# Kernel optimization log

Measured on AMD Instinct MI355X. Metric: run time of the kernel, lower is better.

Reference implementation:

```python
import jax, jax.numpy as jnp
import numpy as np
from jax.ops import segment_sum, segment_max

N_NODES = 100000
N_EDGES = 1600000
IN, HID, OUT = 256, 64, 40
NEG_SLOPE = 0.2  # DGL GATConv default


def setup_inputs() -> dict:
    key = jax.random.key(0)
    ks = jax.random.split(key, 12)
    feat = jax.random.normal(ks[0], (N_NODES, IN), dtype=jnp.float32)
    src = jax.random.randint(ks[1], (N_EDGES,), 0, N_NODES)
    dst = jax.random.randint(ks[2], (N_EDGES,), 0, N_NODES)
    def xavier(k, shape):
        fan = sum(shape)
        return jax.random.normal(k, shape, dtype=jnp.float32) * jnp.sqrt(2.0 / fan)
    return {
        "feat": feat, "src": src, "dst": dst,
        "W1": xavier(ks[3], (IN, HID)),  "b1": jnp.zeros((HID,), jnp.float32),
        "al1": xavier(ks[4], (HID,)),    "ar1": xavier(ks[5], (HID,)),
        "W2": xavier(ks[6], (HID, OUT)), "b2": jnp.zeros((OUT,), jnp.float32),
        "al2": xavier(ks[7], (OUT,)),    "ar2": xavier(ks[8], (OUT,)),
    }


def gat_layer(x, W, b, attn_l, attn_r, src, dst, n):
    # z: [N, F_out] projected features
    z = x @ W
    el = z @ attn_l          # [N] source attention logits
    er = z @ attn_r          # [N] destination attention logits
    e = jax.nn.leaky_relu(el[src] + er[dst], NEG_SLOPE)  # [E]
    # segment (per-destination) softmax over incoming edges
    m = segment_max(e, dst, num_segments=n)              # [N]
    w = jnp.exp(e - m[dst])                              # [E]
    s = segment_sum(w, dst, num_segments=n)              # [N]
    alpha = w / s[dst]                                   # [E]
    # scatter-add aggregation of alpha * z[src]
    out = segment_sum(alpha[:, None] * z[src], dst, num_segments=n)
    return out + b


def reference(feat, src, dst, W1, b1, al1, ar1, W2, b2, al2, ar2):
    n = feat.shape[0]
    h = gat_layer(feat, W1, b1, al1, ar1, src, dst, n)
    h = jax.nn.relu(h)  # dropout is identity in eval mode
    h = gat_layer(h, W2, b2, al2, ar2, src, dst, n)
    return jax.nn.log_softmax(h, axis=-1)  # [N, out_size]
```

## Files before the change

### kernel.cpp

```cpp
#include <hip/hip_runtime.h>
#include <math.h>

constexpr int NN   = 100000;
constexpr int NE   = 1600000;
constexpr int FIN  = 256;
constexpr int HID  = 64;
constexpr int FOUT = 40;
constexpr float SLOPE = 0.2f;
constexpr int NBUCK = (NN + 127) / 128;
constexpr int TILE_A = 2048;
constexpr int NWG_A = (NE + TILE_A - 1) / TILE_A;
constexpr int NT_GEMM = (NN + 63) / 64;
constexpr int AK = 264;
constexpr int HB = 64;
constexpr int HIST_EPB = 4096;
constexpr int NWG_H = (NE + HIST_EPB - 1) / HIST_EPB;

typedef short  short8  __attribute__((ext_vector_type(8)));
typedef float  floatx4 __attribute__((ext_vector_type(4)));

__device__ inline unsigned short f2bf(float x) {
    union { float f; unsigned int u; } c; c.f = x;
    unsigned int u = c.u;
    return (unsigned short)((u + 0x7FFF + ((u >> 16) & 1)) >> 16);
}

__device__ inline float readlane_f(float v, int l) {
    return __int_as_float(__builtin_amdgcn_readlane(__float_as_int(v), l));
}

__device__ inline void scan_buckets(const int* __restrict__ gcnt,
                                    int* __restrict__ bofs,
                                    int* __restrict__ tsum, int t)
{
    int i0 = 4 * t;
    int c0 = (i0 + 0 < NBUCK) ? gcnt[i0 + 0] : 0;
    int c1 = (i0 + 1 < NBUCK) ? gcnt[i0 + 1] : 0;
    int c2 = (i0 + 2 < NBUCK) ? gcnt[i0 + 2] : 0;
    int c3 = (i0 + 3 < NBUCK) ? gcnt[i0 + 3] : 0;
    int s = c0 + c1 + c2 + c3;
    tsum[t] = s;
    __syncthreads();
    for (int off = 1; off < 256; off <<= 1) {
        int x = (t >= off) ? tsum[t - off] : 0;
        __syncthreads();
        tsum[t] += x;
        __syncthreads();
    }
    int e0 = tsum[t] - s;
    if (i0 + 0 <= NBUCK) bofs[i0 + 0] = e0;
    if (i0 + 1 <= NBUCK) bofs[i0 + 1] = e0 + c0;
    if (i0 + 2 <= NBUCK) bofs[i0 + 2] = e0 + c0 + c1;
    if (i0 + 3 <= NBUCK) bofs[i0 + 3] = e0 + c0 + c1 + c2;
    __syncthreads();
}

__global__ __launch_bounds__(256) void prep_kernel(
    const float* __restrict__ W1, unsigned short* __restrict__ W1T,
    const float* __restrict__ W2, const float* __restrict__ al2,
    const float* __restrict__ ar2,
    float* __restrict__ wl2, float* __restrict__ wr2,
    const int* __restrict__ dst, int* __restrict__ bcnt)
{
    const int t = threadIdx.x;
    if (blockIdx.x < HB) {
        int idx = blockIdx.x * 256 + t;
        if (idx < FIN * HID) {
            int k = idx >> 6, n = idx & 63;
            W1T[n * FIN + k] = f2bf(W1[idx]);
        }
        if (blockIdx.x == 0 && t < HID) {
            int k = t;
            float a = 0.f, b = 0.f;
            #pragma unroll 8
            for (int j = 0; j < FOUT; ++j) {
                float wv = W2[k * FOUT + j];
                a += wv * al2[j]; b += wv * ar2[j];
            }
            wl2[k] = a; wr2[k] = b;
        }
    } else {
        __shared__ int hist[NBUCK];
        for (int i = t; i < NBUCK; i += 256) hist[i] = 0;
        __syncthreads();
        int base = (blockIdx.x - HB) * HIST_EPB + t * 16;
        #pragma unroll
        for (int k = 0; k < 4; ++k) {
            int idx = base + 4 * k;
            if (idx < NE) {
                const int4 d4 = *(const int4*)&dst[idx];
                atomicAdd(&hist[d4.x >> 7], 1); atomicAdd(&hist[d4.y >> 7], 1);
                atomicAdd(&hist[d4.z >> 7], 1); atomicAdd(&hist[d4.w >> 7], 1);
            }
        }
        __syncthreads();
        for (int i = t; i < NBUCK; i += 256) {
            int hv = hist[i];
            if (hv) atomicAdd(&bcnt[i], hv);
        }
    }
}

__global__ __launch_bounds__(256) void mega_kernel(
    const float* __restrict__ feat, const unsigned short* __restrict__ W1T,
    const float* __restrict__ al, const float* __restrict__ ar,
    const int* __restrict__ src, const int* __restrict__ dst,
    const int* __restrict__ bcnt, int* __restrict__ cur0,
    int* __restrict__ ebuck,
    _Float16* __restrict__ z, float* __restrict__ el, float* __restrict__ er)
{
    __shared__ int smem4[8448];
    const int t = threadIdx.x;

    if (blockIdx.x < NT_GEMM) {
        unsigned short* sBT = (unsigned short*)smem4;
        const int ntile = blockIdx.x * 64;

        const int w  = t >> 6;
        const int l  = t & 63;
        const int lr = l & 15;
        const int q  = l >> 4;
        const int m0 = 16 * w;

        int n = ntile + m0 + lr; if (n >= NN) n = NN - 1;
        const float* __restrict__ arow = feat + (size_t)n * FIN;

        float4 fa[8], fb[8];
        #pragma unroll
        for (int kc = 0; kc < 8; ++kc) {
            const int koff = kc * 32 + 8 * q;
            fa[kc] = *(const float4*)(arow + koff);
            fb[kc] = *(const float4*)(arow + koff + 4);
        }

        #pragma unroll
        for (int i = 0; i < 8; ++i) {
            int g = t + 256 * i;
            int row = g >> 5, c8 = g & 31;
            *(uint4*)&sBT[row * AK + 8 * c8] = *(const uint4*)&W1T[row * FIN + 8 * c8];
        }
        __syncthreads();

        floatx4 acc[4];
        #pragma unroll
        for (int tile = 0; tile < 4; ++tile) acc[tile] = 0.f;

        #pragma unroll
        for (int kc = 0; kc < 8; ++kc) {
            const int koff = kc * 32 + 8 * q;
            short8 av;
            av[0] = (short)f2bf(fa[kc].x); av[1] = (short)f2bf(fa[kc].y);
            av[2] = (short)f2bf(fa[kc].z); av[3] = (short)f2bf(fa[kc].w);
            av[4] = (short)f2bf(fb[kc].x); av[5] = (short)f2bf(fb[kc].y);
            av[6] = (short)f2bf(fb[kc].z); av[7] = (short)f2bf(fb[kc].w);
            #pragma unroll
            for (int tile = 0; tile < 4; ++tile) {
                const short8 bv = *(const short8*)(sBT + (16 * tile + lr) * AK + koff);
                acc[tile] = __builtin_amdgcn_mfma_f32_16x16x32_bf16(av, bv, acc[tile], 0, 0, 0);
            }
        }

        float aln[4], arn[4];
        #pragma unroll
        for (int tile = 0; tile < 4; ++tile) {
            aln[tile] = al[16 * tile + lr];
            arn[tile] = ar[16 * tile + lr];
        }
        #pragma unroll
        for (int r = 0; r < 4; ++r) {
            int mg = ntile + m0 + 4 * q + r;
            float pl = 0.f, pr = 0.f;
            #pragma unroll
            for (int tile = 0; tile < 4; ++tile) {
                float zv = acc[tile][r];
                pl += zv * aln[tile]; pr += zv * arn[tile];
            }
            #pragma unroll
            for (int off = 8; off >= 1; off >>= 1) {
                pl += __shfl_xor(pl, off);
                pr += __shfl_xor(pr, off);
            }
            if (mg < NN) {
                #pragma unroll
                for (int tile = 0; tile < 4; ++tile)
                    z[(size_t)mg * HID + 16 * tile + lr] = (_Float16)acc[tile][r];
                if (lr == 0) { el[mg] = pl; er[mg] = pr; }
            }
        }
    } else {
        int* hist = smem4;
        int* bofs = smem4 + NBUCK;
        int* tsum = smem4 + 2 * NBUCK + 1;
        int* lcur = smem4 + 2 * NBUCK + 1 + 256;
        const int blk = blockIdx.x - NT_GEMM;
        const int e0 = blk * TILE_A;
        const int e1 = (e0 + TILE_A < NE) ? e0 + TILE_A : NE;

        for (int i = t; i < NBUCK; i += 256) hist[i] = 0;
        scan_buckets(bcnt, bofs, tsum, t);
        for (int e = e0 + t; e < e1; e += 256)
            atomicAdd(&hist[dst[e] >> 7], 1);
        __syncthreads();
        for (int i = t; i < NBUCK; i += 256) {
            int hv = hist[i];
            if (hv) lcur[i] = bofs[i] + atomicAdd(&cur0[i], hv);
        }
        __syncthreads();
        for (int e = e0 + t; e < e1; e += 256) {
            int d = dst[e], s_ = src[e];
            int p = atomicAdd(&lcur[d >> 7], 1);
            ebuck[p] = (s_ << 7) | (d & 127);
        }
    }
}

__global__ __launch_bounds__(256) void partB_kernel(
    const int* __restrict__ bcnt, const int* __restrict__ ebuck,
    int* __restrict__ row_ptr, int* __restrict__ esrc)
{
    __shared__ int bofs[NBUCK + 1];
    __shared__ int tsum[256];
    __shared__ int sdeg[128];
    __shared__ int sscan[128];
    __shared__ int scur[128];
    const int b = blockIdx.x;
    const int n0 = b << 7;
    const int t = threadIdx.x;

    if (t < 128) sdeg[t] = 0;
    scan_buckets(bcnt, bofs, tsum, t);
    const int r0 = bofs[b], r1 = bofs[b + 1];

    for (int e = r0 + t; e < r1; e += 256)
        atomicAdd(&sdeg[ebuck[e] & 127], 1);
    __syncthreads();

    if (t < 128) sscan[t] = sdeg[t];
    __syncthreads();
    for (int off = 1; off < 128; off <<= 1) {
        int x = (t < 128 && t >= off) ? sscan[t - off] : 0;
        __syncthreads();
        if (t < 128) sscan[t] += x;
        __syncthreads();
    }
    if (t < 128) {
        int excl = sscan[t] - sdeg[t];
        if (n0 + t < NN) row_ptr[n0 + t] = r0 + excl;
        scur[t] = r0 + excl;
    }
    if (b == NBUCK - 1 && t == 0) row_ptr[NN] = NE;
    __syncthreads();

    for (int e = r0 + t; e < r1; e += 256) {
        int pk = ebuck[e];
        int p = atomicAdd(&scur[pk & 127], 1);
        esrc[p] = pk >> 7;
    }
}

template<bool FIRST>
__global__ __launch_bounds__(256) void gat_gather_kernel(
    const int* __restrict__ row_ptr, const int* __restrict__ esrc,
    const float* __restrict__ el, const float* __restrict__ er,
    const _Float16* __restrict__ zin, const float* __restrict__ b1,
    const float* __restrict__ wl2, const float* __restrict__ wr2,
    _Float16* __restrict__ hout, _Float16* __restrict__ haggout,
    float* __restrict__ el2, float* __restrict__ er2)
{
    const int w = threadIdx.x >> 6, lane = threadIdx.x & 63;
    const int d = blockIdx.x * 4 + w;
    const int r0 = row_ptr[d], r1 = row_ptr[d + 1];
    const int cnt = r1 - r0;
    const float erd = er[d];

    float accv = 0.f;
    float s = 0.f;

    if (cnt <= 64) {
        int sn = 0; float v = -INFINITY;
        if (lane < cnt) {
            sn = esrc[r0 + lane];
            v = el[sn] + erd;
            v = (v >= 0.f) ? v : SLOPE * v;
        }
        float m = v;
        #pragma unroll
        for (int off = 32; off >= 1; off >>= 1) m = fmaxf(m, __shfl_xor(m, off));
        float wv = (lane < cnt) ? __expf(v - m) : 0.f;
        s = wv;
        #pragma unroll
        for (int off = 32; off >= 1; off >>= 1) s += __shfl_xor(s, off);
        {
            int j = 0;
            for (; j + 8 <= cnt; j += 8) {
                float a0 = 0.f, a1 = 0.f;
                #pragma unroll
                for (int qq = 0; qq < 8; qq += 2) {
                    float w0 = readlane_f(wv, j + qq);
                    int   s0 = __builtin_amdgcn_readlane(sn, j + qq);
                    float w1 = readlane_f(wv, j + qq + 1);
                    int   s1 = __builtin_amdgcn_readlane(sn, j + qq + 1);
                    a0 += w0 * (float)zin[(size_t)s0 * HID + lane];
                    a1 += w1 * (float)zin[(size_t)s1 * HID + lane];
                }
                accv += a0 + a1;
            }
            for (; j < cnt; ++j) {
                float w0 = readlane_f(wv, j);
                int   s0 = __builtin_amdgcn_readlane(sn, j);
                accv += w0 * (float)zin[(size_t)s0 * HID + lane];
            }
        }
    } else {
        float m = -INFINITY;
        for (int e = r0 + lane; e < r1; e += 64) {
            float v = el[esrc[e]] + erd;
            v = (v >= 0.f) ? v : SLOPE * v;
            m = fmaxf(m, v);
        }
        #pragma unroll
        for (int off = 32; off >= 1; off >>= 1) m = fmaxf(m, __shfl_xor(m, off));
        for (int base = r0; base < r1; base += 64) {
            int e = base + lane;
            float wv = 0.f; int sn = 0;
            if (e < r1) {
                sn = esrc[e];
                float v = el[sn] + erd;
                v = (v >= 0.f) ? v : SLOPE * v;
                wv = __expf(v - m);
            }
            s += wv;
            int c = r1 - base; if (c > 64) c = 64;
            {
                int j = 0;
                for (; j + 4 <= c; j += 4) {
                    float a0 = 0.f, a1 = 0.f;
                    #pragma unroll
                    for (int qq = 0; qq < 4; qq += 2) {
                        float w0 = readlane_f(wv, j + qq);
                        int   s0 = __builtin_amdgcn_readlane(sn, j + qq);
                        float w1 = readlane_f(wv, j + qq + 1);
                        int   s1 = __builtin_amdgcn_readlane(sn, j + qq + 1);
                        a0 += w0 * (float)zin[(size_t)s0 * HID + lane];
                        a1 += w1 * (float)zin[(size_t)s1 * HID + lane];
                    }
                    accv += a0 + a1;
                }
                for (; j < c; ++j) {
                    float w0 = readlane_f(wv, j);
                    int   s0 = __builtin_amdgcn_readlane(sn, j);
                    accv += w0 * (float)zin[(size_t)s0 * HID + lane];
                }
            }
        }
        #pragma unroll
        for (int off = 32; off >= 1; off >>= 1) s += __shfl_xor(s, off);
    }

    float res = (cnt > 0) ? (accv / s) : 0.f;

    if (FIRST) {
        float hval = res + b1[lane];
        hval = (hval > 0.f) ? hval : 0.f;
        hout[(size_t)d * HID + lane] = (_Float16)hval;
        float pl = hval * wl2[lane];
        float pr = hval * wr2[lane];
        #pragma unroll
        for (int off = 32; off >= 1; off >>= 1) {
            pl += __shfl_xor(pl, off); pr += __shfl_xor(pr, off);
        }
        if (lane == 0) { el2[d] = pl; er2[d] = pr; }
    } else {
        haggout[(size_t)d * HID + lane] = (_Float16)res;
    }
}

__global__ __launch_bounds__(256) void out_kernel(
    const _Float16* __restrict__ hagg, const float* __restrict__ W2,
    const float* __restrict__ b2, float* __restrict__ out)
{
    __shared__ float sh[4][64];
    const int w = threadIdx.x >> 6, lane = threadIdx.x & 63;
    const int n = blockIdx.x * 4 + w;
    sh[w][lane] = (float)hagg[(size_t)n * HID + lane];
    __syncthreads();
    float acc = 0.f;
    if (lane < FOUT) {
        #pragma unroll 8
        for (int k = 0; k < HID; ++k) acc += sh[w][k] * W2[k * FOUT + lane];
    }
    float v = (lane < FOUT) ? acc + b2[lane] : -INFINITY;
    float mx = v;
    #pragma unroll
    for (int off = 32; off >= 1; off >>= 1) mx = fmaxf(mx, __shfl_xor(mx, off));
    float ex = (lane < FOUT) ? __expf(v - mx) : 0.f;
    float sm = ex;
    #pragma unroll
    for (int off = 32; off >= 1; off >>= 1) sm += __shfl_xor(sm, off);
    if (lane < FOUT) out[(size_t)n * FOUT + lane] = v - mx - __logf(sm);
}

extern "C" void kernel_launch(void* const* d_in, const int* in_sizes, int n_in,
                              void* d_out, int out_size, void* d_ws, size_t ws_size,
                              hipStream_t stream) {
    const float* feat = (const float*)d_in[0];
    const int*   src  = (const int*)d_in[1];
    const int*   dst  = (const int*)d_in[2];
    const float* W1   = (const float*)d_in[3];
    const float* b1   = (const float*)d_in[4];
    const float* al1  = (const float*)d_in[5];
    const float* ar1  = (const float*)d_in[6];
    const float* W2   = (const float*)d_in[7];
    const float* b2   = (const float*)d_in[8];
    const float* al2  = (const float*)d_in[9];
    const float* ar2  = (const float*)d_in[10];
    float* out = (float*)d_out;

    char* p = (char*)d_ws;
    _Float16* hagg = (_Float16*)p;
    _Float16* z1   = (_Float16*)p;  p += (size_t)NN * HID * 2;
    _Float16* h    = (_Float16*)p;  p += (size_t)NN * HID * 2;
    float* el1   = (float*)p;     p += (size_t)NN * 4;
    float* er1   = (float*)p;     p += (size_t)NN * 4;
    float* el2   = (float*)p;     p += (size_t)NN * 4;
    float* er2   = (float*)p;     p += (size_t)NN * 4;
    float* wl2   = (float*)p;     p += HID * 4;
    float* wr2   = (float*)p;     p += HID * 4;
    int*   bcnt  = (int*)p;       p += NBUCK * 4;
    int*   cur0  = (int*)p;       p += NBUCK * 4;
    int*   rowp  = (int*)p;       p += (NN + 1) * 4;
    int*   esrc  = (int*)p;       p += (size_t)NE * 4;
    int*   ebuck = (int*)p;       p += (size_t)NE * 4;
    unsigned short* w1t = (unsigned short*)p;

    hipMemsetAsync(bcnt, 0, 2 * NBUCK * sizeof(int), stream);

    prep_kernel<<<HB + NWG_H, 256, 0, stream>>>(
        W1, w1t, W2, al2, ar2, wl2, wr2, dst, bcnt);

    mega_kernel<<<NT_GEMM + NWG_A, 256, 0, stream>>>(
        feat, w1t, al1, ar1, src, dst, bcnt, cur0, ebuck, z1, el1, er1);

    partB_kernel<<<NBUCK, 256, 0, stream>>>(bcnt, ebuck, rowp, esrc);

    gat_gather_kernel<true><<<NN / 4, 256, 0, stream>>>(
        rowp, esrc, el1, er1, z1, b1, wl2, wr2, h, nullptr, el2, er2);

    gat_gather_kernel<false><<<NN / 4, 256, 0, stream>>>(
        rowp, esrc, el2, er2, h, nullptr, nullptr, nullptr,
        nullptr, hagg, nullptr, nullptr);

    out_kernel<<<NN / 4, 256, 0, stream>>>(hagg, W2, b2, out);
}
```

Before: 419.7 us.

## Double GEMM rows per workgroup in fused kernel to amortize W1 LDS staging

Each GEMM workgroup now processes 128 nodes instead of 64, computing two sets of MFMA accumulators that share the same W1 B-fragment loaded from LDS. This halves the number of W1 staging copies and GEMM blocks, and the feat loads are now interleaved with compute per k-chunk rather than all prefetched up front. The trade-off is fewer GEMM blocks, which lowers parallelism, and more accumulator registers per thread. The lcur write is also made unconditional, a minor branch cleanup.

After: 417.4 us. Within noise of the previous version (-0.5%).

```diff
diff --git a/kernel.cpp b/kernel.cpp
--- a/kernel.cpp
+++ b/kernel.cpp
@@ -10,7 +10,7 @@
 constexpr int NBUCK = (NN + 127) / 128;
 constexpr int TILE_A = 2048;
 constexpr int NWG_A = (NE + TILE_A - 1) / TILE_A;
-constexpr int NT_GEMM = (NN + 63) / 64;
+constexpr int NT_GEMM = (NN + 127) / 128;
 constexpr int AK = 264;
 constexpr int HB = 64;
 constexpr int HIST_EPB = 4096;
@@ -114,7 +114,15 @@
 
     if (blockIdx.x < NT_GEMM) {
         unsigned short* sBT = (unsigned short*)smem4;
-        const int ntile = blockIdx.x * 64;
+        const int ntile = blockIdx.x * 128;
+
+        #pragma unroll
+        for (int i = 0; i < 8; ++i) {
+            int g = t + 256 * i;
+            int row = g >> 5, c8 = g & 31;
+            *(uint4*)&sBT[row * AK + 8 * c8] = *(const uint4*)&W1T[row * FIN + 8 * c8];
+        }
+        __syncthreads();
 
         const int w  = t >> 6;
         const int l  = t & 63;
@@ -122,41 +130,36 @@
         const int q  = l >> 4;
         const int m0 = 16 * w;
 
-        int n = ntile + m0 + lr; if (n >= NN) n = NN - 1;
-        const float* __restrict__ arow = feat + (size_t)n * FIN;
-
-        float4 fa[8], fb[8];
+        int n1 = ntile + m0 + lr; if (n1 >= NN) n1 = NN - 1;
+        int n2 = ntile + 64 + m0 + lr; if (n2 >= NN) n2 = NN - 1;
+        const float* __restrict__ arow1 = feat + (size_t)n1 * FIN;
+        const float* __restrict__ arow2 = feat + (size_t)n2 * FIN;
+
+        floatx4 acc1[4], acc2[4];
+        #pragma unroll
+        for (int tile = 0; tile < 4; ++tile) { acc1[tile] = 0.f; acc2[tile] = 0.f; }
+
         #pragma unroll
         for (int kc = 0; kc < 8; ++kc) {
             const int koff = kc * 32 + 8 * q;
-            fa[kc] = *(const float4*)(arow + koff);
-            fb[kc] = *(const float4*)(arow + koff + 4);
-        }
-
-        #pragma unroll
-        for (int i = 0; i < 8; ++i) {
-            int g = t + 256 * i;
-            int row = g >> 5, c8 = g & 31;
-            *(uint4*)&sBT[row * AK + 8 * c8] = *(const uint4*)&W1T[row * FIN + 8 * c8];
-        }
-        __syncthreads();
-
-        floatx4 acc[4];
-        #pragma unroll
-        for (int tile = 0; tile < 4; ++tile) acc[tile] = 0.f;
-
-        #pragma unroll
-        for (int kc = 0; kc < 8; ++kc) {
-            const int koff = kc * 32 + 8 * q;
-            short8 av;
-            av[0] = (short)f2bf(fa[kc].x); av[1] = (short)f2bf(fa[kc].y);
-            av[2] = (short)f2bf(fa[kc].z); av[3] = (short)f2bf(fa[kc].w);
-            av[4] = (short)f2bf(fb[kc].x); av[5] = (short)f2bf(fb[kc].y);
-            av[6] = (short)f2bf(fb[kc].z); av[7] = (short)f2bf(fb[kc].w);
+            const float4 fa1 = *(const float4*)(arow1 + koff);
+            const float4 fb1 = *(const float4*)(arow1 + koff + 4);
+            const float4 fa2 = *(const float4*)(arow2 + koff);
+            const float4 fb2 = *(const float4*)(arow2 + koff + 4);
+            short8 av1, av2;
+            av1[0] = (short)f2bf(fa1.x); av1[1] = (short)f2bf(fa1.y);
+            av1[2] = (short)f2bf(fa1.z); av1[3] = (short)f2bf(fa1.w);
+            av1[4] = (short)f2bf(fb1.x); av1[5] = (short)f2bf(fb1.y);
+            av1[6] = (short)f2bf(fb1.z); av1[7] = (short)f2bf(fb1.w);
+            av2[0] = (short)f2bf(fa2.x); av2[1] = (short)f2bf(fa2.y);
+            av2[2] = (short)f2bf(fa2.z); av2[3] = (short)f2bf(fa2.w);
+            av2[4] = (short)f2bf(fb2.x); av2[5] = (short)f2bf(fb2.y);
+            av2[6] = (short)f2bf(fb2.z); av2[7] = (short)f2bf(fb2.w);
             #pragma unroll
             for (int tile = 0; tile < 4; ++tile) {
                 const short8 bv = *(const short8*)(sBT + (16 * tile + lr) * AK + koff);
-                acc[tile] = __builtin_amdgcn_mfma_f32_16x16x32_bf16(av, bv, acc[tile], 0, 0, 0);
+                acc1[tile] = __builtin_amdgcn_mfma_f32_16x16x32_bf16(av1, bv, acc1[tile], 0, 0, 0);
+                acc2[tile] = __builtin_amdgcn_mfma_f32_16x16x32_bf16(av2, bv, acc2[tile], 0, 0, 0);
             }
         }
 
@@ -168,23 +171,31 @@
         }
         #pragma unroll
         for (int r = 0; r < 4; ++r) {
-            int mg = ntile + m0 + 4 * q + r;
-            float pl = 0.f, pr = 0.f;
+            int mg1 = ntile + m0 + 4 * q + r;
+            int mg2 = mg1 + 64;
+            float pl1 = 0.f, pr1 = 0.f, pl2 = 0.f, pr2 = 0.f;
             #pragma unroll
             for (int tile = 0; tile < 4; ++tile) {
-                float zv = acc[tile][r];
-                pl += zv * aln[tile]; pr += zv * arn[tile];
+                float z1v = acc1[tile][r], z2v = acc2[tile][r];
+                pl1 += z1v * aln[tile]; pr1 += z1v * arn[tile];
+                pl2 += z2v * aln[tile]; pr2 += z2v * arn[tile];
             }
             #pragma unroll
             for (int off = 8; off >= 1; off >>= 1) {
-                pl += __shfl_xor(pl, off);
-                pr += __shfl_xor(pr, off);
-            }
-            if (mg < NN) {
+                pl1 += __shfl_xor(pl1, off); pr1 += __shfl_xor(pr1, off);
+                pl2 += __shfl_xor(pl2, off); pr2 += __shfl_xor(pr2, off);
+            }
+            if (mg1 < NN) {
                 #pragma unroll
                 for (int tile = 0; tile < 4; ++tile)
-                    z[(size_t)mg * HID + 16 * tile + lr] = (_Float16)acc[tile][r];
-                if (lr == 0) { el[mg] = pl; er[mg] = pr; }
+                    z[(size_t)mg1 * HID + 16 * tile + lr] = (_Float16)acc1[tile][r];
+                if (lr == 0) { el[mg1] = pl1; er[mg1] = pr1; }
+            }
+            if (mg2 < NN) {
+                #pragma unroll
+                for (int tile = 0; tile < 4; ++tile)
+                    z[(size_t)mg2 * HID + 16 * tile + lr] = (_Float16)acc2[tile][r];
+                if (lr == 0) { el[mg2] = pl2; er[mg2] = pr2; }
             }
         }
     } else {
@@ -203,7 +214,7 @@
         __syncthreads();
         for (int i = t; i < NBUCK; i += 256) {
             int hv = hist[i];
-            if (hv) lcur[i] = bofs[i] + atomicAdd(&cur0[i], hv);
+            lcur[i] = hv ? (bofs[i] + atomicAdd(&cur0[i], hv)) : 0;
         }
         __syncthreads();
         for (int e = e0 + t; e < e1; e += 256) {
```
